# Optimization experiments

Hardware: AMD Instinct MI355X
Metric: run time of the kernel (lower is better)

The kernel has to match this reference:

```python
import jax, jax.numpy as jnp
import numpy as np

B, N, T, D, H = 4, 8, 512, 256, 8
DK = D // H


def _dwconv(x, w, b=None):
    # x: (BN, D, T) depthwise conv, kernel 3, padding 'same', groups=D
    y = jax.lax.conv_general_dilated(
        x, w, window_strides=(1,), padding='SAME',
        feature_group_count=x.shape[1],
        dimension_numbers=('NCH', 'OIH', 'NCH'))
    if b is not None:
        y = y + b[None, :, None]
    return y


def setup_inputs() -> dict:
    key = jax.random.key(0)
    ks = jax.random.split(key, 16)
    s = 1.0 / np.sqrt(D)
    s3 = 1.0 / np.sqrt(3 * D)
    inp = {
        'query': jax.random.normal(ks[0], (B, N, T, D), jnp.float32),
        'key': jax.random.normal(ks[1], (B, N, T, D), jnp.float32),
        'value': jax.random.normal(ks[2], (B, N, T, D), jnp.float32),
        'key_padding_mask': jax.random.randint(ks[3], (B, N, T), 0, 2, jnp.int32),
        # depthwise conv params
        'w_pos': jax.random.uniform(ks[4], (D, 1, 3), jnp.float32, -0.577, 0.577),
        'b_pos': jax.random.uniform(ks[5], (D,), jnp.float32, -0.577, 0.577),
        # physics-initialized differential operators (still learnable floats)
        'w_vel': jnp.tile(jnp.array([-1.0, 0.0, 1.0], jnp.float32)[None, None, :], (D, 1, 1)),
        'w_acc': jnp.tile(jnp.array([1.0, -2.0, 1.0], jnp.float32)[None, None, :], (D, 1, 1)),
        # fusion / projection linears (stored as (in, out))
        'Wq': jax.random.uniform(ks[6], (3 * D, D), jnp.float32, -s3, s3),
        'bq': jax.random.uniform(ks[7], (D,), jnp.float32, -s3, s3),
        'Wk': jax.random.uniform(ks[8], (3 * D, D), jnp.float32, -s3, s3),
        'bk': jax.random.uniform(ks[9], (D,), jnp.float32, -s3, s3),
        'Wv': jax.random.uniform(ks[10], (D, D), jnp.float32, -s, s),
        'bv': jax.random.uniform(ks[11], (D,), jnp.float32, -s, s),
        'Wo': jax.random.uniform(ks[12], (D, D), jnp.float32, -s, s),
        'bo': jax.random.uniform(ks[13], (D,), jnp.float32, -s, s),
    }
    return inp


def reference(query, key, value, key_padding_mask,
              w_pos, b_pos, w_vel, w_acc,
              Wq, bq, Wk, bk, Wv, bv, Wo, bo):
    b, n, t, d = query.shape
    scale = jnp.float32(1.0 / np.sqrt(DK))

    def kin_feats(x):
        xin = x.reshape(b * n, t, d).transpose(0, 2, 1)  # (BN, D, T)
        p = _dwconv(xin, w_pos, b_pos)
        v = _dwconv(xin, w_vel)
        a = _dwconv(xin, w_acc)
        return jnp.concatenate([p, v, a], axis=1).transpose(0, 2, 1)  # (BN, T, 3D)

    qc = kin_feats(query)
    kc = kin_feats(key)

    Q = (qc @ Wq + bq).reshape(b, n, t, H, DK).transpose(0, 1, 3, 2, 4)  # (B,N,H,Tq,dk)
    K = (kc @ Wk + bk).reshape(b, n, t, H, DK).transpose(0, 1, 3, 2, 4)
    V = (value @ Wv + bv).reshape(b, n, t, H, DK).transpose(0, 1, 3, 2, 4)

    scores = jnp.einsum('bnhqd,bnhkd->bnhqk', Q, K) * scale
    mask = key_padding_mask.astype(bool)[:, :, None, None, :]  # (B,N,1,1,Tk)
    scores = jnp.where(mask, jnp.float32(-1e9), scores)
    attn = jax.nn.softmax(scores, axis=-1)  # dropout is identity in eval

    ctx = jnp.einsum('bnhqk,bnhkd->bnhqd', attn, V)
    ctx = ctx.transpose(0, 1, 3, 2, 4).reshape(b, n, t, d)
    return ctx @ Wo + bo
```

## Files before the change

### kernel.cpp

```cpp
#include <hip/hip_runtime.h>
#include <math.h>


typedef __attribute__((ext_vector_type(8))) short bf16x8;
typedef __attribute__((ext_vector_type(4))) float f32x4;
typedef __attribute__((ext_vector_type(16))) float f32x16;
typedef __attribute__((ext_vector_type(4))) int i32x4;

__device__ __forceinline__ unsigned short f2bf(float f) {
    unsigned u = __float_as_uint(f);
    return (unsigned short)((u + 0x7fff + ((u >> 16) & 1)) >> 16);
}
__device__ __forceinline__ float ex2(float x) {
    float r; asm("v_exp_f32 %0, %1" : "=v"(r) : "v"(x)); return r;
}
__device__ __forceinline__ int cvtpk(float lo, float hi) {
    int r; asm("v_cvt_pk_bf16_f32 %0, %1, %2" : "=v"(r) : "v"(lo), "v"(hi)); return r;
}
__device__ __forceinline__ void gll16(const void* gsrc, const void* ldst) {
    __builtin_amdgcn_global_load_lds(
        (const __attribute__((address_space(1))) unsigned int*)gsrc,
        (__attribute__((address_space(3))) unsigned int*)ldst, 16, 0, 0);
}

#define SCL (0.17677669529663689f * 1.4426950408889634f)

#define OFF_XPQ  0u
#define OFF_XPK  8421376u
#define OFF_VB   16842752u
#define OFF_BTQ  25231360u
#define OFF_BTK  25624576u
#define OFF_BEFF 26017792u
#define OFF_WVT  26019840u
#define OFF_WOT  26150912u
#define OFF_QB   26413056u
#define OFF_KB   34801664u
#define OFF_VV   43190272u
#define OFF_CTX  51578880u

__global__ __launch_bounds__(256) void cvtprep(
    const float* __restrict__ q, const float* __restrict__ k, const float* __restrict__ v,
    unsigned short* __restrict__ xpq, unsigned short* __restrict__ xpk,
    unsigned short* __restrict__ vb,
    const float* __restrict__ Wq, const float* __restrict__ Wk,
    const float* __restrict__ bq, const float* __restrict__ bk,
    const float* __restrict__ wp, const float* __restrict__ wv,
    const float* __restrict__ wa, const float* __restrict__ b_pos,
    const float* __restrict__ Wv, const float* __restrict__ Wo,
    unsigned short* __restrict__ BtQ, unsigned short* __restrict__ BtK,
    float* __restrict__ beff, unsigned short* __restrict__ WVT,
    unsigned short* __restrict__ WOT)
{
    int bid = blockIdx.x;
    if (bid < 4112) {
        int idx = bid * 256 + threadIdx.x;
        int which = idx / 526336;
        int r = idx - which * 526336;
        int bn = r / 16448;
        int rr = r - bn * 16448;
        int p = rr >> 5;
        int c8 = (rr & 31) * 8;
        const float* src = which ? k : q;
        unsigned short* dst = which ? xpk : xpq;
        unsigned o[4] = {0, 0, 0, 0};
        if (p != 0 && p != 513) {
            const float* s = src + ((size_t)(bn * 512 + p - 1) * 256 + c8);
            float4 a = *(const float4*)s;
            float4 b = *(const float4*)(s + 4);
            o[0] = f2bf(a.x) | ((unsigned)f2bf(a.y) << 16);
            o[1] = f2bf(a.z) | ((unsigned)f2bf(a.w) << 16);
            o[2] = f2bf(b.x) | ((unsigned)f2bf(b.y) << 16);
            o[3] = f2bf(b.z) | ((unsigned)f2bf(b.w) << 16);
        }
        unsigned* d = (unsigned*)(dst + ((size_t)(bn * 514 + p) * 256 + c8));
        d[0] = o[0]; d[1] = o[1]; d[2] = o[2]; d[3] = o[3];
    } else if (bid < 6160) {
        int idx = (bid - 4112) * 256 + threadIdx.x;
        int row = idx >> 5;
        int c8 = (idx & 31) * 8;
        const float* s = v + ((size_t)row * 256 + c8);
        float4 a = *(const float4*)s;
        float4 b = *(const float4*)(s + 4);
        unsigned* d = (unsigned*)(vb + ((size_t)row * 256 + c8));
        d[0] = f2bf(a.x) | ((unsigned)f2bf(a.y) << 16);
        d[1] = f2bf(a.z) | ((unsigned)f2bf(a.w) << 16);
        d[2] = f2bf(b.x) | ((unsigned)f2bf(b.y) << 16);
        d[3] = f2bf(b.z) | ((unsigned)f2bf(b.w) << 16);
    } else if (bid < 7696) {
        int idx = (bid - 6160) * 256 + threadIdx.x;
        int which = idx / 196608;
        int r = idx - which * 196608;
        int j = r >> 16;
        int rem = r & 65535;
        int n = rem >> 8;
        int d = rem & 255;
        const float* W = which ? Wk : Wq;
        float val = wp[d * 3 + j] * W[d * 256 + n]
                  + wv[d * 3 + j] * W[(256 + d) * 256 + n]
                  + wa[d * 3 + j] * W[(512 + d) * 256 + n];
        if (!which) val *= SCL;
        (which ? BtK : BtQ)[n * 768 + j * 256 + d] = f2bf(val);
    } else if (bid < 8208) {
        int idx = (bid - 7696) * 256 + threadIdx.x;
        int which = idx >> 16;
        int r = idx & 65535;
        int n = r >> 8, kk = r & 255;
        if (!which) WVT[n * 256 + kk] = f2bf(Wv[kk * 256 + n]);
        else        WOT[n * 256 + kk] = f2bf(Wo[kk * 256 + n]);
    } else {
        int which = bid - 8208;
        int n = threadIdx.x;
        const float* W = which ? Wk : Wq;
        const float* bb = which ? bk : bq;
        float s = bb[n];
        for (int d = 0; d < 256; ++d) s = fmaf(b_pos[d], W[d * 256 + n], s);
        if (!which) s *= SCL;
        beff[which * 256 + n] = s;
    }
}

template<int KTOT, bool IM2COL, typename OutT>
__device__ __forceinline__ void gemm97(
    const unsigned short* __restrict__ A, const unsigned short* __restrict__ Bt,
    const float* __restrict__ bias, OutT* __restrict__ Out,
    unsigned short* As, unsigned short* Bs)
{
    const int tid = threadIdx.x;
    const int wid = tid >> 6, l = tid & 63;
    const int l31 = l & 31, h2 = l >> 5;
    const int wm = wid >> 1, wn = wid & 1;
    const int m0 = blockIdx.x * 128, n0 = blockIdx.y * 128;

    f32x16 acc[2][2] = {};

    for (int k0 = 0; k0 < KTOT; k0 += 64) {
        __syncthreads();
        #pragma unroll
        for (int q = 0; q < 4; ++q) {
            int cidx = q * 256 + wid * 64 + l;
            int row = cidx >> 3;
            int csrc = ((cidx & 7) ^ (row & 7)) * 8;
            const unsigned short* asrc;
            if constexpr (IM2COL) {
                int seq = m0 >> 9, t0 = m0 & 511;
                asrc = A + ((size_t)(seq * 514 + t0 + row + (k0 >> 8)) * 256 + (k0 & 255) + csrc);
            } else {
                asrc = A + ((size_t)(m0 + row) * 256 + (k0 & 255) + csrc);
            }
            gll16(asrc, As + (q * 256 + wid * 64) * 8);
            gll16(Bt + (size_t)(n0 + row) * KTOT + k0 + csrc, Bs + (q * 256 + wid * 64) * 8);
        }
        __syncthreads();
        #pragma unroll
        for (int ks = 0; ks < 4; ++ks) {
            bf16x8 af[2], bfr[2];
            #pragma unroll
            for (int mt = 0; mt < 2; ++mt) {
                int r = wm * 64 + mt * 32 + l31;
                af[mt] = *(const bf16x8*)&As[r * 64 + (((ks * 2 + h2) ^ (r & 7)) * 8)];
            }
            #pragma unroll
            for (int nt = 0; nt < 2; ++nt) {
                int rn = wn * 64 + nt * 32 + l31;
                bfr[nt] = *(const bf16x8*)&Bs[rn * 64 + (((ks * 2 + h2) ^ (rn & 7)) * 8)];
            }
            #pragma unroll
            for (int mt = 0; mt < 2; ++mt)
                #pragma unroll
                for (int nt = 0; nt < 2; ++nt)
                    acc[mt][nt] = __builtin_amdgcn_mfma_f32_32x32x16_bf16(af[mt], bfr[nt], acc[mt][nt], 0, 0, 0);
        }
    }

    #pragma unroll
    for (int nt = 0; nt < 2; ++nt) {
        const int col = n0 + wn * 64 + nt * 32 + l31;
        const float bb = bias[col];
        #pragma unroll
        for (int mt = 0; mt < 2; ++mt) {
            #pragma unroll
            for (int r = 0; r < 16; ++r) {
                const int row = m0 + wm * 64 + mt * 32 + 4 * h2 + (r & 3) + 8 * (r >> 2);
                float v = acc[mt][nt][r] + bb;
                if constexpr (sizeof(OutT) == 2) Out[(size_t)row * 256 + col] = (OutT)f2bf(v);
                else Out[(size_t)row * 256 + col] = v;
            }
        }
    }
}

__global__ __launch_bounds__(256) void proj_fused(
    const unsigned short* __restrict__ XPQ, const unsigned short* __restrict__ XPK,
    const unsigned short* __restrict__ VB,
    const unsigned short* __restrict__ BTQ, const unsigned short* __restrict__ BTK,
    const unsigned short* __restrict__ WVT,
    const float* __restrict__ BEFF, const float* __restrict__ bv,
    unsigned short* __restrict__ QB, unsigned short* __restrict__ KB,
    unsigned short* __restrict__ VV)
{
    __shared__ alignas(16) unsigned short As[8192];
    __shared__ alignas(16) unsigned short Bs[8192];
    const int z = blockIdx.z;
    if (z == 0)      gemm97<768, true, unsigned short>(XPQ, BTQ, BEFF, QB, As, Bs);
    else if (z == 1) gemm97<768, true, unsigned short>(XPK, BTK, BEFF + 256, KB, As, Bs);
    else             gemm97<256, false, unsigned short>(VB, WVT, bv, VV, As, Bs);
}

__global__ __launch_bounds__(256) void outproj(
    const unsigned short* __restrict__ CTX, const unsigned short* __restrict__ WOT,
    const float* __restrict__ bo, float* __restrict__ Out)
{
    __shared__ alignas(16) unsigned short As[8192];
    __shared__ alignas(16) unsigned short Bs[8192];
    gemm97<256, false, float>(CTX, WOT, bo, Out, As, Bs);
}

__global__ __launch_bounds__(512) void attn_mfma(const unsigned short* __restrict__ Qb,
                                                 const unsigned short* __restrict__ Kb,
                                                 const unsigned short* __restrict__ Vv,
                                                 const int* __restrict__ mask,
                                                 unsigned short* __restrict__ ctx) {
    __shared__ alignas(16) unsigned short Qs[128 * 32];
    __shared__ alignas(16) unsigned short Ks[2][128 * 32];
    __shared__ alignas(16) unsigned short VsT[2][32 * 136];
    __shared__ float Mb[2][128];

    const int qt = blockIdx.x, bnh = blockIdx.y;
    const int bn = bnh >> 3, h = bnh & 7;
    const int tid = threadIdx.x, wid = tid >> 6, l = tid & 63;
    const int g = l >> 4, r15 = l & 15;
    const unsigned short* Qg = Qb + (size_t)bn * 512 * 256 + h * 32;
    const unsigned short* Kg = Kb + (size_t)bn * 512 * 256 + h * 32;
    const unsigned short* Vg = Vv + (size_t)bn * 512 * 256 + h * 32;
    const int* mp = mask + bn * 512;
    const int srow = tid >> 2;
    const int vkey = tid & 127, vd0 = (tid >> 7) * 8;

    auto stageK = [&](int k0, int b) {
        int csrc = (((tid & 3) ^ (srow & 3))) * 8;
        gll16(Kg + ((size_t)(k0 + srow)) * 256 + csrc, &Ks[b][wid * 512]);
    };

    gll16(Qg + ((size_t)(qt * 128 + srow)) * 256 + (tid & 3) * 8, Qs + wid * 512);
    stageK(0, 0);
    {
        i32x4 vr = *(const i32x4*)(const void*)(Vg + (size_t)vkey * 256 + vd0);
        #pragma unroll
        for (int i = 0; i < 4; ++i) {
            unsigned u = (unsigned)vr[i];
            VsT[0][(vd0 + 2 * i) * 136 + vkey] = (unsigned short)(u & 0xffff);
            VsT[0][(vd0 + 2 * i + 1) * 136 + vkey] = (unsigned short)(u >> 16);
        }
        if (tid < 128) Mb[0][tid] = (mp[tid] != 0) ? -1e9f : 0.f;
    }
    __syncthreads();

    const bf16x8 bq = *(const bf16x8*)&Qs[(wid * 16 + r15) * 32 + g * 8];

    float mrun = -1e30f, lrun = 0.f;
    f32x4 accO[2] = {};

    for (int kt = 0; kt < 4; ++kt) {
        const int cur = kt & 1, nxt = cur ^ 1;
        const int k0n = kt * 128 + 128;

        i32x4 vr;
        int mraw = 0;
        if (kt < 3) {
            stageK(k0n, nxt);
            vr = *(const i32x4*)(const void*)(Vg + ((size_t)(k0n + vkey)) * 256 + vd0);
            if (tid < 128) mraw = mp[k0n + tid];
        }

        float p[8][4];
        float rmax = -3e38f;
        __builtin_amdgcn_s_setprio(1);
        #pragma unroll
        for (int t2 = 0; t2 < 8; ++t2) {
            const int base = 32 * (t2 >> 1) + 4 * (t2 & 1);
            const int arow = base + 8 * (r15 >> 2) + (r15 & 3);
            bf16x8 ak = *(const bf16x8*)&Ks[cur][arow * 32 + ((g ^ (arow & 3)) * 8)];
            f32x4 cin = *(const f32x4*)&Mb[cur][base + 8 * g];
            f32x4 st = __builtin_amdgcn_mfma_f32_16x16x32_bf16(ak, bq, cin, 0, 0, 0);
            #pragma unroll
            for (int r = 0; r < 4; ++r) p[t2][r] = st[r];
            rmax = fmaxf(rmax, fmaxf(fmaxf(st[0], st[1]), fmaxf(st[2], st[3])));
        }
        __builtin_amdgcn_s_setprio(0);
        rmax = fmaxf(rmax, __shfl_xor(rmax, 16, 64));
        rmax = fmaxf(rmax, __shfl_xor(rmax, 32, 64));

        if (__ballot(rmax > mrun)) {
            float mnew = fmaxf(mrun, rmax);
            float fs = ex2(mrun - mnew);
            lrun *= fs;
            accO[0] *= fs;
            accO[1] *= fs;
            mrun = mnew;
        }
        float psum = 0.f;
        #pragma unroll
        for (int t2 = 0; t2 < 8; ++t2)
            #pragma unroll
            for (int r = 0; r < 4; ++r) {
                float e = ex2(p[t2][r] - mrun);
                p[t2][r] = e;
                psum += e;
            }
        psum += __shfl_xor(psum, 16, 64);
        psum += __shfl_xor(psum, 32, 64);
        lrun += psum;

        bf16x8 pb[4];
        #pragma unroll
        for (int s = 0; s < 4; ++s) {
            i32x4 bi = {cvtpk(p[2 * s][0], p[2 * s][1]), cvtpk(p[2 * s][2], p[2 * s][3]),
                        cvtpk(p[2 * s + 1][0], p[2 * s + 1][1]), cvtpk(p[2 * s + 1][2], p[2 * s + 1][3])};
            pb[s] = __builtin_bit_cast(bf16x8, bi);
        }

        __builtin_amdgcn_s_setprio(1);
        #pragma unroll
        for (int mt = 0; mt < 2; ++mt)
            #pragma unroll
            for (int s = 0; s < 4; ++s) {
                bf16x8 av = *(const bf16x8*)&VsT[cur][(mt * 16 + r15) * 136 + 32 * s + 8 * g];
                accO[mt] = __builtin_amdgcn_mfma_f32_16x16x32_bf16(av, pb[s], accO[mt], 0, 0, 0);
            }
        __builtin_amdgcn_s_setprio(0);

        if (kt < 3) {
            #pragma unroll
            for (int i = 0; i < 4; ++i) {
                unsigned u = (unsigned)vr[i];
                VsT[nxt][(vd0 + 2 * i) * 136 + vkey] = (unsigned short)(u & 0xffff);
                VsT[nxt][(vd0 + 2 * i + 1) * 136 + vkey] = (unsigned short)(u >> 16);
            }
            if (tid < 128) Mb[nxt][tid] = (mraw != 0) ? -1e9f : 0.f;
        }
        __syncthreads();
    }

    const float inv = 1.f / lrun;
    const size_t orow = (size_t)bn * 512 + qt * 128 + wid * 16 + r15;
    #pragma unroll
    for (int mt = 0; mt < 2; ++mt) {
        ushort4 o;
        o.x = f2bf(accO[mt][0] * inv);
        o.y = f2bf(accO[mt][1] * inv);
        o.z = f2bf(accO[mt][2] * inv);
        o.w = f2bf(accO[mt][3] * inv);
        *(ushort4*)&ctx[orow * 256 + h * 32 + mt * 16 + 4 * g] = o;
    }
}

extern "C" void kernel_launch(void* const* d_in, const int* in_sizes, int n_in,
                              void* d_out, int out_size, void* d_ws, size_t ws_size,
                              hipStream_t stream) {
    const float* query = (const float*)d_in[0];
    const float* key   = (const float*)d_in[1];
    const float* value = (const float*)d_in[2];
    const int*   kpm   = (const int*)d_in[3];
    const float* w_pos = (const float*)d_in[4];
    const float* b_pos = (const float*)d_in[5];
    const float* w_vel = (const float*)d_in[6];
    const float* w_acc = (const float*)d_in[7];
    const float* Wq    = (const float*)d_in[8];
    const float* bq    = (const float*)d_in[9];
    const float* Wk    = (const float*)d_in[10];
    const float* bk    = (const float*)d_in[11];
    const float* Wv    = (const float*)d_in[12];
    const float* bv    = (const float*)d_in[13];
    const float* Wo    = (const float*)d_in[14];
    const float* bo    = (const float*)d_in[15];

    unsigned char* w = (unsigned char*)d_ws;
    unsigned short* XPQ = (unsigned short*)(w + OFF_XPQ);
    unsigned short* XPK = (unsigned short*)(w + OFF_XPK);
    unsigned short* VB  = (unsigned short*)(w + OFF_VB);
    unsigned short* BTQ = (unsigned short*)(w + OFF_BTQ);
    unsigned short* BTK = (unsigned short*)(w + OFF_BTK);
    float*          BEFF= (float*)(w + OFF_BEFF);
    unsigned short* WVT = (unsigned short*)(w + OFF_WVT);
    unsigned short* WOT = (unsigned short*)(w + OFF_WOT);
    unsigned short* QB  = (unsigned short*)(w + OFF_QB);
    unsigned short* KB  = (unsigned short*)(w + OFF_KB);
    unsigned short* VV  = (unsigned short*)(w + OFF_VV);
    unsigned short* CTX = (unsigned short*)(w + OFF_CTX);

    cvtprep<<<8210, 256, 0, stream>>>(query, key, value, XPQ, XPK, VB,
                                      Wq, Wk, bq, bk, w_pos, w_vel, w_acc, b_pos,
                                      Wv, Wo, BTQ, BTK, BEFF, WVT, WOT);

    proj_fused<<<dim3(128, 2, 3), 256, 0, stream>>>(XPQ, XPK, VB, BTQ, BTK, WVT,
                                                    BEFF, bv, QB, KB, VV);

    attn_mfma<<<dim3(4, 256), 512, 0, stream>>>(QB, KB, VV, kpm, CTX);

    outproj<<<dim3(128, 2), 256, 0, stream>>>(CTX, WOT, bo, (float*)d_out);
}
```

Measured before the change: 91.90 us.

## Process all four query tiles per block to reuse staged K/V

```diff
diff --git a/kernel.cpp b/kernel.cpp
--- a/kernel.cpp
+++ b/kernel.cpp
@@ -220,12 +220,12 @@
                                                  const unsigned short* __restrict__ Vv,
                                                  const int* __restrict__ mask,
                                                  unsigned short* __restrict__ ctx) {
-    __shared__ alignas(16) unsigned short Qs[128 * 32];
+    __shared__ alignas(16) unsigned short Qs[512 * 32];
     __shared__ alignas(16) unsigned short Ks[2][128 * 32];
     __shared__ alignas(16) unsigned short VsT[2][32 * 136];
     __shared__ float Mb[2][128];
 
-    const int qt = blockIdx.x, bnh = blockIdx.y;
+    const int bnh = blockIdx.x;
     const int bn = bnh >> 3, h = bnh & 7;
     const int tid = threadIdx.x, wid = tid >> 6, l = tid & 63;
     const int g = l >> 4, r15 = l & 15;
@@ -241,7 +241,12 @@
         gll16(Kg + ((size_t)(k0 + srow)) * 256 + csrc, &Ks[b][wid * 512]);
     };
 
-    gll16(Qg + ((size_t)(qt * 128 + srow)) * 256 + (tid & 3) * 8, Qs + wid * 512);
+    #pragma unroll
+    for (int q = 0; q < 4; ++q) {
+        int chunk = q * 512 + tid;
+        int row = chunk >> 2, c = chunk & 3;
+        gll16(Qg + (size_t)row * 256 + c * 8, Qs + (q * 512 + wid * 64) * 8);
+    }
     stageK(0, 0);
     {
         i32x4 vr = *(const i32x4*)(const void*)(Vg + (size_t)vkey * 256 + vd0);
@@ -255,10 +260,15 @@
     }
     __syncthreads();
 
-    const bf16x8 bq = *(const bf16x8*)&Qs[(wid * 16 + r15) * 32 + g * 8];
-
-    float mrun = -1e30f, lrun = 0.f;
-    f32x4 accO[2] = {};
+    bf16x8 bq[4];
+    #pragma unroll
+    for (int qt = 0; qt < 4; ++qt)
+        bq[qt] = *(const bf16x8*)&Qs[(qt * 128 + wid * 16 + r15) * 32 + g * 8];
+
+    float mrun[4], lrun[4];
+    f32x4 accO[4][2] = {};
+    #pragma unroll
+    for (int qt = 0; qt < 4; ++qt) { mrun[qt] = -1e30f; lrun[qt] = 0.f; }
 
     for (int kt = 0; kt < 4; ++kt) {
         const int cur = kt & 1, nxt = cur ^ 1;
@@ -272,62 +282,70 @@
             if (tid < 128) mraw = mp[k0n + tid];
         }
 
-        float p[8][4];
-        float rmax = -3e38f;
-        __builtin_amdgcn_s_setprio(1);
-        #pragma unroll
-        for (int t2 = 0; t2 < 8; ++t2) {
-            const int base = 32 * (t2 >> 1) + 4 * (t2 & 1);
-            const int arow = base + 8 * (r15 >> 2) + (r15 & 3);
-            bf16x8 ak = *(const bf16x8*)&Ks[cur][arow * 32 + ((g ^ (arow & 3)) * 8)];
-            f32x4 cin = *(const f32x4*)&Mb[cur][base + 8 * g];
-            f32x4 st = __builtin_amdgcn_mfma_f32_16x16x32_bf16(ak, bq, cin, 0, 0, 0);
-            #pragma unroll
-            for (int r = 0; r < 4; ++r) p[t2][r] = st[r];
-            rmax = fmaxf(rmax, fmaxf(fmaxf(st[0], st[1]), fmaxf(st[2], st[3])));
-        }
-        __builtin_amdgcn_s_setprio(0);
-        rmax = fmaxf(rmax, __shfl_xor(rmax, 16, 64));
-        rmax = fmaxf(rmax, __shfl_xor(rmax, 32, 64));
-
-        if (__ballot(rmax > mrun)) {
-            float mnew = fmaxf(mrun, rmax);
-            float fs = ex2(mrun - mnew);
-            lrun *= fs;
-            accO[0] *= fs;
-            accO[1] *= fs;
-            mrun = mnew;
-        }
-        float psum = 0.f;
-        #pragma unroll
-        for (int t2 = 0; t2 < 8; ++t2)
-            #pragma unroll
-            for (int r = 0; r < 4; ++r) {
-                float e = ex2(p[t2][r] - mrun);
-                p[t2][r] = e;
-                psum += e;
-            }
-        psum += __shfl_xor(psum, 16, 64);
-        psum += __shfl_xor(psum, 32, 64);
-        lrun += psum;
-
-        bf16x8 pb[4];
-        #pragma unroll
-        for (int s = 0; s < 4; ++s) {
-            i32x4 bi = {cvtpk(p[2 * s][0], p[2 * s][1]), cvtpk(p[2 * s][2], p[2 * s][3]),
-                        cvtpk(p[2 * s + 1][0], p[2 * s + 1][1]), cvtpk(p[2 * s + 1][2], p[2 * s + 1][3])};
-            pb[s] = __builtin_bit_cast(bf16x8, bi);
-        }
-
-        __builtin_amdgcn_s_setprio(1);
+        bf16x8 av[2][4];
         #pragma unroll
         for (int mt = 0; mt < 2; ++mt)
             #pragma unroll
+            for (int s = 0; s < 4; ++s)
+                av[mt][s] = *(const bf16x8*)&VsT[cur][(mt * 16 + r15) * 136 + 32 * s + 8 * g];
+
+        #pragma unroll
+        for (int qt = 0; qt < 4; ++qt) {
+            float p[8][4];
+            float rmax = -3e38f;
+            __builtin_amdgcn_s_setprio(1);
+            #pragma unroll
+            for (int t2 = 0; t2 < 8; ++t2) {
+                const int base = 32 * (t2 >> 1) + 4 * (t2 & 1);
+                const int arow = base + 8 * (r15 >> 2) + (r15 & 3);
+                bf16x8 ak = *(const bf16x8*)&Ks[cur][arow * 32 + ((g ^ (arow & 3)) * 8)];
+                f32x4 cin = *(const f32x4*)&Mb[cur][base + 8 * g];
+                f32x4 st = __builtin_amdgcn_mfma_f32_16x16x32_bf16(ak, bq[qt], cin, 0, 0, 0);
+                #pragma unroll
+                for (int r = 0; r < 4; ++r) p[t2][r] = st[r];
+                rmax = fmaxf(rmax, fmaxf(fmaxf(st[0], st[1]), fmaxf(st[2], st[3])));
+            }
+            __builtin_amdgcn_s_setprio(0);
+            rmax = fmaxf(rmax, __shfl_xor(rmax, 16, 64));
+            rmax = fmaxf(rmax, __shfl_xor(rmax, 32, 64));
+
+            if (__ballot(rmax > mrun[qt])) {
+                float mnew = fmaxf(mrun[qt], rmax);
+                float fs = ex2(mrun[qt] - mnew);
+                lrun[qt] *= fs;
+                accO[qt][0] *= fs;
+                accO[qt][1] *= fs;
+                mrun[qt] = mnew;
+            }
+            float psum = 0.f;
+            #pragma unroll
+            for (int t2 = 0; t2 < 8; ++t2)
+                #pragma unroll
+                for (int r = 0; r < 4; ++r) {
+                    float e = ex2(p[t2][r] - mrun[qt]);
+                    p[t2][r] = e;
+                    psum += e;
+                }
+            psum += __shfl_xor(psum, 16, 64);
+            psum += __shfl_xor(psum, 32, 64);
+            lrun[qt] += psum;
+
+            bf16x8 pb[4];
+            #pragma unroll
             for (int s = 0; s < 4; ++s) {
-                bf16x8 av = *(const bf16x8*)&VsT[cur][(mt * 16 + r15) * 136 + 32 * s + 8 * g];
-                accO[mt] = __builtin_amdgcn_mfma_f32_16x16x32_bf16(av, pb[s], accO[mt], 0, 0, 0);
-            }
-        __builtin_amdgcn_s_setprio(0);
+                i32x4 bi = {cvtpk(p[2 * s][0], p[2 * s][1]), cvtpk(p[2 * s][2], p[2 * s][3]),
+                            cvtpk(p[2 * s + 1][0], p[2 * s + 1][1]), cvtpk(p[2 * s + 1][2], p[2 * s + 1][3])};
+                pb[s] = __builtin_bit_cast(bf16x8, bi);
+            }
+
+            __builtin_amdgcn_s_setprio(1);
+            #pragma unroll
+            for (int mt = 0; mt < 2; ++mt)
+                #pragma unroll
+                for (int s = 0; s < 4; ++s)
+                    accO[qt][mt] = __builtin_amdgcn_mfma_f32_16x16x32_bf16(av[mt][s], pb[s], accO[qt][mt], 0, 0, 0);
+            __builtin_amdgcn_s_setprio(0);
+        }
 
         if (kt < 3) {
             #pragma unroll
@@ -341,16 +359,19 @@
         __syncthreads();
     }
 
-    const float inv = 1.f / lrun;
-    const size_t orow = (size_t)bn * 512 + qt * 128 + wid * 16 + r15;
     #pragma unroll
-    for (int mt = 0; mt < 2; ++mt) {
-        ushort4 o;
-        o.x = f2bf(accO[mt][0] * inv);
-        o.y = f2bf(accO[mt][1] * inv);
-        o.z = f2bf(accO[mt][2] * inv);
-        o.w = f2bf(accO[mt][3] * inv);
-        *(ushort4*)&ctx[orow * 256 + h * 32 + mt * 16 + 4 * g] = o;
+    for (int qt = 0; qt < 4; ++qt) {
+        const float inv = 1.f / lrun[qt];
+        const size_t orow = (size_t)bn * 512 + qt * 128 + wid * 16 + r15;
+        #pragma unroll
+        for (int mt = 0; mt < 2; ++mt) {
+            ushort4 o;
+            o.x = f2bf(accO[qt][mt][0] * inv);
+            o.y = f2bf(accO[qt][mt][1] * inv);
+            o.z = f2bf(accO[qt][mt][2] * inv);
+            o.w = f2bf(accO[qt][mt][3] * inv);
+            *(ushort4*)&ctx[orow * 256 + h * 32 + mt * 16 + 4 * g] = o;
+        }
     }
 }
 
@@ -395,7 +416,7 @@
     proj_fused<<<dim3(128, 2, 3), 256, 0, stream>>>(XPQ, XPK, VB, BTQ, BTK, WVT,
                                                     BEFF, bv, QB, KB, VV);
 
-    attn_mfma<<<dim3(4, 256), 512, 0, stream>>>(QB, KB, VV, kpm, CTX);
+    attn_mfma<<<256, 512, 0, stream>>>(QB, KB, VV, kpm, CTX);
 
     outproj<<<dim3(128, 2), 256, 0, stream>>>(CTX, WOT, bo, (float*)d_out);
 }
```

Result: faster. 88.21 us (-4.0%).
